# Kernel optimization log

Measured on AMD Instinct MI355X. Metric: run time of the kernel, lower is better.

Reference implementation:

```python
import jax, jax.numpy as jnp
import numpy as np
import math

IMAGE_SIZE = 256
VIEWING_ANGLE = 30.0  # degrees
NEAR = 0.1
FAR = 100.0
CHUNK = 50


def _look_at(vertices):
    # nr.look_at with at=origin, up=+y, eye from viewing_angle (as in __init__)
    eye = jnp.array([0.0, 0.0, -(1.0 / math.tan(math.radians(VIEWING_ANGLE)) + 1.0)],
                    dtype=vertices.dtype)
    at = jnp.zeros(3, dtype=vertices.dtype)
    up = jnp.array([0.0, 1.0, 0.0], dtype=vertices.dtype)
    z = at - eye
    z = z / jnp.linalg.norm(z)
    x = jnp.cross(up, z)
    x = x / jnp.linalg.norm(x)
    y = jnp.cross(z, x)
    y = y / jnp.linalg.norm(y)
    R = jnp.stack([x, y, z])  # [3,3] rows = camera axes
    return (vertices - eye) @ R.T


def _perspective(v):
    # nr.perspective: x,y divided by z*tan(angle); z (camera depth) kept
    width = math.tan(math.radians(VIEWING_ANGLE))
    z = v[..., 2]
    zs = jnp.where(jnp.abs(z) < 1e-5, 1e-5, z)  # avoid div-by-zero for behind-camera verts
    return jnp.stack([v[..., 0] / (zs * width), v[..., 1] / (zs * width), z], axis=-1)


def reference(vertices, faces):
    """Renderer.forward(vertices, faces, mode='depth'):
    fill_back -> look_at -> perspective -> vertices_to_faces -> rasterize_depth.
    Returns depth image [B, H, W] (FAR where no face covers the pixel)."""
    B = vertices.shape[0]
    # fill_back: append faces with reversed vertex order
    faces2 = jnp.concatenate([faces, faces[:, :, ::-1]], axis=1)  # [B, 2F, 3]
    v_scr = _perspective(_look_at(vertices))                      # [B, V, 3]
    # vertices_to_faces gather
    fv = jax.vmap(lambda v, f: v[f])(v_scr, faces2)               # [B, 2F, 3, 3]
    F2 = fv.shape[1]
    nsteps = F2 // CHUNK
    fv = fv.reshape(B, nsteps, CHUNK, 3, 3).transpose(1, 0, 2, 3, 4)  # [S,B,C,3,3]

    is_ = IMAGE_SIZE
    p = (2.0 * jnp.arange(is_, dtype=vertices.dtype) + 1.0 - is_) / is_  # pixel centers in (-1,1)
    py, px = jnp.meshgrid(p, p, indexing='ij')  # [H,W]

    def step(buf, f):  # f: [B,C,3,3]; z-buffer min over this face chunk
        x = f[..., 0][..., None, None]  # [B,C,3,1,1]
        y = f[..., 1][..., None, None]
        z = f[..., 2]                   # [B,C,3] camera-space depth per vertex
        x0, x1, x2 = x[:, :, 0], x[:, :, 1], x[:, :, 2]
        y0, y1, y2 = y[:, :, 0], y[:, :, 1], y[:, :, 2]
        area = (x1 - x0) * (y2 - y0) - (x2 - x0) * (y1 - y0)  # [B,C,1,1] signed 2*area
        area_s = jnp.where(jnp.abs(area) < 1e-8, 1e-8, area)
        # screen-space barycentric weights (edge functions / area)
        w0 = ((x1 - px) * (y2 - py) - (x2 - px) * (y1 - py)) / area_s
        w1 = ((x2 - px) * (y0 - py) - (x0 - px) * (y2 - py)) / area_s
        w2 = 1.0 - w0 - w1
        zc = jnp.maximum(z, 1e-4)  # safe for masked-out faces only
        # perspective-correct depth: z = 1 / (w0/z0 + w1/z1 + w2/z2)
        inv_z = (w0 / zc[:, :, 0, None, None] + w1 / zc[:, :, 1, None, None]
                 + w2 / zc[:, :, 2, None, None])
        zp = 1.0 / jnp.maximum(inv_z, 1e-6)
        front = jnp.all(z > NEAR, axis=-1)[..., None, None]
        inside = (w0 >= 0) & (w1 >= 0) & (w2 >= 0) & (jnp.abs(area) > 1e-8)
        valid = inside & front & (zp > NEAR) & (zp < FAR)
        zp = jnp.where(valid, zp, FAR)
        return jnp.minimum(buf, jnp.min(zp, axis=1)), None

    buf0 = jnp.full((B, is_, is_), FAR, dtype=vertices.dtype)
    depth, _ = jax.lax.scan(step, buf0, fv)
    return depth


def setup_inputs() -> dict:
    key = jax.random.key(0)
    kv, kf = jax.random.split(key)
    B, NV, NF = 1, 2502, 5000
    # mesh roughly within the camera frustum (eye at z~-2.73 looking at origin)
    vertices = 0.35 * jax.random.normal(kv, (B, NV, 3), dtype=jnp.float32)
    faces = jax.random.randint(kf, (B, NF, 3), 0, NV, dtype=jnp.int32)
    return {"vertices": vertices, "faces": faces}
```

## Files before the change

kernel.cpp:

```cpp
#include <hip/hip_runtime.h>
#include <hip/hip_bf16.h>

#define IS 256
#define NEARV 0.1f
#define FARV 100.0f
#define NTX 16
#define NTILES 256
#define CAP 5120
#define CHK 32
#define CPT ((CAP + CHK - 1) / CHK)
#define RBLOCKS 2048
#define RWAVES (RBLOCKS * 4)
#define MAXITEMS (NTILES * CPT)

__global__ void kinit(unsigned int* __restrict__ zb, int* __restrict__ count,
                      int* __restrict__ misc) {
    int i = blockIdx.x * 256 + threadIdx.x;
    zb[i] = 0x42C80000u;
    if (i < NTILES) count[i] = 0;
    if (i == NTILES) misc[0] = 0;
}

__launch_bounds__(256)
__global__ void kbinprep(const float* __restrict__ verts, const int* __restrict__ faces,
                         float4* __restrict__ fd, int* __restrict__ count,
                         unsigned short* __restrict__ list, int* __restrict__ misc,
                         int* __restrict__ items, int nf) {
    __shared__ int scnt[NTILES];
    __shared__ int sbase[NTILES];
    __shared__ int slast;
    const int tid = threadIdx.x;
    for (int t = tid; t < NTILES; t += 256) scnt[t] = 0;
    __syncthreads();

    const int f = blockIdx.x * 256 + tid;
    int kx0 = 0, kx1 = -1, ky0 = 0, ky1 = -1;
    float bxmin = 0.f, bymin = 0.f, bxmax = -1.f, bymax = -1.f;
    if (f < nf) {
        int i0 = faces[f * 3 + 0];
        int i1 = faces[f * 3 + 1];
        int i2 = faces[f * 3 + 2];
        float z0 = verts[i0 * 3 + 2] + 2.7320508075688772f;
        float z1 = verts[i1 * 3 + 2] + 2.7320508075688772f;
        float z2 = verts[i2 * 3 + 2] + 2.7320508075688772f;
        bool front = (z0 > NEARV) && (z1 > NEARV) && (z2 > NEARV);
        float zs0 = (fabsf(z0) < 1e-5f) ? 1e-5f : z0;
        float zs1 = (fabsf(z1) < 1e-5f) ? 1e-5f : z1;
        float zs2 = (fabsf(z2) < 1e-5f) ? 1e-5f : z2;
        float d0 = zs0 * 0.57735026918962576f;
        float d1 = zs1 * 0.57735026918962576f;
        float d2 = zs2 * 0.57735026918962576f;
        float x0 = verts[i0 * 3 + 0] / d0;
        float y0 = verts[i0 * 3 + 1] / d0;
        float x1 = verts[i1 * 3 + 0] / d1;
        float y1 = verts[i1 * 3 + 1] / d1;
        float x2 = verts[i2 * 3 + 0] / d2;
        float y2 = verts[i2 * 3 + 1] / d2;
        float area = (x1 - x0) * (y2 - y0) - (x2 - x0) * (y1 - y0);
        if (front && (fabsf(area) > 1e-8f)) {
            float xmin = fminf(x0, fminf(x1, x2));
            float xmax = fmaxf(x0, fmaxf(x1, x2));
            float ymin = fminf(y0, fminf(y1, y2));
            float ymax = fmaxf(y0, fmaxf(y1, y2));
            float ia = 1.0f / area;
            float iz0 = 1.0f / fmaxf(z0, 1e-4f);
            float iz1 = 1.0f / fmaxf(z1, 1e-4f);
            float iz2 = 1.0f / fmaxf(z2, 1e-4f);
            float4* o = fd + (size_t)f * 4;
            o[0] = make_float4(x0, y0, x1, y1);
            o[1] = make_float4(x2, y2, ia, iz0);
            o[2] = make_float4(iz1, iz2, 0.0f, 0.0f);
            bxmin = xmin; bymin = ymin; bxmax = xmax; bymax = ymax;
            float tminx = fminf(fmaxf((bxmin * 256.0f + 225.0f) * (1.0f / 32.0f), -2.0f), 17.0f);
            float tmaxx = fminf(fmaxf((bxmax * 256.0f + 255.0f) * (1.0f / 32.0f), -2.0f), 17.0f);
            float tminy = fminf(fmaxf((bymin * 256.0f + 225.0f) * (1.0f / 32.0f), -2.0f), 17.0f);
            float tmaxy = fminf(fmaxf((bymax * 256.0f + 255.0f) * (1.0f / 32.0f), -2.0f), 17.0f);
            kx0 = max(0, (int)ceilf(tminx) - 1);
            kx1 = min(NTX - 1, (int)floorf(tmaxx) + 1);
            ky0 = max(0, (int)ceilf(tminy) - 1);
            ky1 = min(NTX - 1, (int)floorf(tmaxy) + 1);
        }
    }
    for (int ky = ky0; ky <= ky1; ++ky) {
        float py_lo = (float)(32 * ky - 255) * (1.0f / 256.0f);
        float py_hi = (float)(32 * ky - 225) * (1.0f / 256.0f);
        if (!(bymin <= py_hi && bymax >= py_lo)) continue;
        for (int kx = kx0; kx <= kx1; ++kx) {
            float px_lo = (float)(32 * kx - 255) * (1.0f / 256.0f);
            float px_hi = (float)(32 * kx - 225) * (1.0f / 256.0f);
            if (bxmin <= px_hi && bxmax >= px_lo) atomicAdd(&scnt[ky * NTX + kx], 1);
        }
    }
    __syncthreads();
    for (int t = tid; t < NTILES; t += 256) {
        int c = scnt[t];
        sbase[t] = (c > 0) ? atomicAdd(&count[t], c) : 0;
        scnt[t] = 0;
    }
    __syncthreads();
    for (int ky = ky0; ky <= ky1; ++ky) {
        float py_lo = (float)(32 * ky - 255) * (1.0f / 256.0f);
        float py_hi = (float)(32 * ky - 225) * (1.0f / 256.0f);
        if (!(bymin <= py_hi && bymax >= py_lo)) continue;
        for (int kx = kx0; kx <= kx1; ++kx) {
            float px_lo = (float)(32 * kx - 255) * (1.0f / 256.0f);
            float px_hi = (float)(32 * kx - 225) * (1.0f / 256.0f);
            if (bxmin <= px_hi && bxmax >= px_lo) {
                int t = ky * NTX + kx;
                int slot = sbase[t] + atomicAdd(&scnt[t], 1);
                list[(size_t)t * CAP + slot] = (unsigned short)f;
            }
        }
    }
    __syncthreads();
    __threadfence();
    if (tid == 0) slast = (atomicAdd(&misc[0], 1) == (int)gridDim.x - 1) ? 1 : 0;
    __syncthreads();
    if (!slast) return;
    __threadfence();
    int c = __hip_atomic_load(&count[tid], __ATOMIC_RELAXED, __HIP_MEMORY_SCOPE_AGENT);
    int nch = (c + CHK - 1) / CHK;
    scnt[tid] = nch;
    __syncthreads();
    for (int d = 1; d < NTILES; d <<= 1) {
        int v = (tid >= d) ? scnt[tid - d] : 0;
        __syncthreads();
        scnt[tid] += v;
        __syncthreads();
    }
    int off = scnt[tid] - nch;
    if (tid == NTILES - 1) misc[64] = scnt[tid];
    for (int k = 0; k < nch; ++k) {
        int n = min(CHK, c - k * CHK);
        items[off + k] = (tid << 16) | (n << 8) | k;
    }
}

__launch_bounds__(256)
__global__ void kraster(const float4* __restrict__ fd, const unsigned int* __restrict__ list32,
                        const int* __restrict__ items, const int* __restrict__ misc,
                        unsigned int* __restrict__ zb) {
    const int wslot = __builtin_amdgcn_readfirstlane(threadIdx.x >> 6);
    const int wid = blockIdx.x * 4 + wslot;
    const int lane = threadIdx.x & 63;
    const int cx = lane & 15;
    const int ry = lane >> 4;
    const int ni = __builtin_amdgcn_readfirstlane(misc[64]);

    for (int it = wid; it < ni; it += RWAVES) {
        const int pk = __builtin_amdgcn_readfirstlane(items[it]);
        const int tile = pk >> 16;
        const int n = (pk >> 8) & 0xff;
        const int chunk = pk & 0xff;
        const int bx = tile & 15;
        const int by = tile >> 4;
        const int j = bx * 16 + cx;
        const float px = ((float)(2 * j + 1) - 256.0f) * (1.0f / 256.0f);
        float py[4];
        int row[4];
        unsigned int zcur[4];
#pragma unroll
        for (int r = 0; r < 4; ++r) {
            row[r] = by * 16 + ry + 4 * r;
            py[r] = ((float)(2 * row[r] + 1) - 256.0f) * (1.0f / 256.0f);
            zcur[r] = zb[row[r] * IS + j];
        }
        const unsigned int* lp32 = list32 + ((size_t)tile * CAP + chunk * CHK) / 2;

        float mx[4] = {0.0f, 0.0f, 0.0f, 0.0f};
        unsigned int pr = 0;

#pragma unroll 2
        for (int e = 0; e < n; ++e) {
            if ((e & 1) == 0)
                pr = (unsigned int)__builtin_amdgcn_readfirstlane((int)lp32[e >> 1]);
            const int fidx = (e & 1) ? (int)(pr >> 16) : (int)(pr & 0xffffu);
            const float4* p = fd + (size_t)fidx * 4;
            float4 a0 = p[0];
            float4 a1 = p[1];
            float4 a2 = p[2];
            float dx0 = a0.x - px, dx1 = a0.z - px, dx2 = a1.x - px;
#pragma unroll
            for (int r = 0; r < 4; ++r) {
                float dy0 = a0.y - py[r], dy1 = a0.w - py[r], dy2 = a1.y - py[r];
                float e0 = dx1 * dy2 - dx2 * dy1;
                float e1 = dx2 * dy0 - dx0 * dy2;
                float w0 = e0 * a1.z;
                float w1 = e1 * a1.z;
                float w2 = 1.0f - w0 - w1;
                float invz = w0 * a1.w + w1 * a2.x + w2 * a2.y;
                float invzc = fmaxf(invz, 1e-6f);
                float wmin = fminf(fminf(w0, w1), w2);
                bool ok = (wmin >= 0.0f) && (invzc < 10.0f) && (invzc > 0.01f);
                if (ok) mx[r] = fmaxf(mx[r], invzc);
            }
        }
#pragma unroll
        for (int r = 0; r < 4; ++r) {
            if (mx[r] > 0.0f) {
                float zp = 1.0f / mx[r];
                unsigned int zbits = __float_as_uint(zp);
                if (zbits < zcur[r]) atomicMin(&zb[row[r] * IS + j], zbits);
            }
        }
    }
}

extern "C" void kernel_launch(void* const* d_in, const int* in_sizes, int n_in,
                              void* d_out, int out_size, void* d_ws, size_t ws_size,
                              hipStream_t stream) {
    const float* verts = (const float*)d_in[0];
    const int* faces = (const int*)d_in[1];
    unsigned int* zb = (unsigned int*)d_out;

    const int nf = in_sizes[1] / 3;

    char* ws = (char*)d_ws;
    size_t off = 0;
    float4* fd = (float4*)(ws + off);            off += (size_t)nf * 64;
    off = (off + 255) & ~(size_t)255;
    int* count = (int*)(ws + off);               off += NTILES * 4;
    off = (off + 255) & ~(size_t)255;
    int* misc = (int*)(ws + off);                off += 512;
    int* items = (int*)(ws + off);               off += (size_t)MAXITEMS * 4;
    off = (off + 255) & ~(size_t)255;
    unsigned short* list = (unsigned short*)(ws + off);

    const int nb = (nf + 255) / 256;

    kinit<<<(IS * IS) / 256, 256, 0, stream>>>(zb, count, misc);
    kbinprep<<<nb, 256, 0, stream>>>(verts, faces, fd, count, list, misc, items, nf);
    kraster<<<RBLOCKS, 256, 0, stream>>>(fd, (const unsigned int*)list, items, misc, zb);
}
```

Baseline: 110.9 us.

## Replace global atomics and last-block scan with per-segment bin lists

Merges the z-buffer init kernel into the prep kernel and drops the global per-tile atomic counters, the last-block detection and the prefix scan that built the work-item list. Each block now writes its per-tile counts to a tile×segment table and fills a fixed 256-entry slot region per segment. The raster kernel then walks a fixed grid of tile×slot work units, with an XOR swizzle, and skips empty ones. This removes one launch and the serialized tail in binning, at the cost of scanning many empty work slots and using sparser list storage.

```diff
diff --git a/kernel.cpp b/kernel.cpp
--- a/kernel.cpp
+++ b/kernel.cpp
@@ -1,39 +1,33 @@
 #include <hip/hip_runtime.h>
-#include <hip/hip_bf16.h>
 
 #define IS 256
 #define NEARV 0.1f
 #define FARV 100.0f
 #define NTX 16
 #define NTILES 256
-#define CAP 5120
+#define SEGSZ 256
+#define NSEGMAX 20
+#define CAP (SEGSZ * NSEGMAX)
 #define CHK 32
-#define CPT ((CAP + CHK - 1) / CHK)
 #define RBLOCKS 2048
 #define RWAVES (RBLOCKS * 4)
-#define MAXITEMS (NTILES * CPT)
-
-__global__ void kinit(unsigned int* __restrict__ zb, int* __restrict__ count,
-                      int* __restrict__ misc) {
-    int i = blockIdx.x * 256 + threadIdx.x;
-    zb[i] = 0x42C80000u;
-    if (i < NTILES) count[i] = 0;
-    if (i == NTILES) misc[0] = 0;
-}
+#define NSLOTS (NTILES * 256)
 
 __launch_bounds__(256)
-__global__ void kbinprep(const float* __restrict__ verts, const int* __restrict__ faces,
-                         float4* __restrict__ fd, int* __restrict__ count,
-                         unsigned short* __restrict__ list, int* __restrict__ misc,
-                         int* __restrict__ items, int nf) {
+__global__ void kprep(const float* __restrict__ verts, const int* __restrict__ faces,
+                      float4* __restrict__ fd, int* __restrict__ cnt2,
+                      unsigned short* __restrict__ list, unsigned int* __restrict__ zb,
+                      int nf, int nseg) {
     __shared__ int scnt[NTILES];
-    __shared__ int sbase[NTILES];
-    __shared__ int slast;
     const int tid = threadIdx.x;
-    for (int t = tid; t < NTILES; t += 256) scnt[t] = 0;
+    const int bid = blockIdx.x;
+    zb[bid * 256 + tid] = 0x42C80000u;
+    if (bid >= nseg) return;
+
+    scnt[tid] = 0;
     __syncthreads();
 
-    const int f = blockIdx.x * 256 + tid;
+    const int f = bid * 256 + tid;
     int kx0 = 0, kx1 = -1, ky0 = 0, ky1 = -1;
     float bxmin = 0.f, bymin = 0.f, bxmax = -1.f, bymax = -1.f;
     if (f < nf) {
@@ -58,10 +52,10 @@
         float y2 = verts[i2 * 3 + 1] / d2;
         float area = (x1 - x0) * (y2 - y0) - (x2 - x0) * (y1 - y0);
         if (front && (fabsf(area) > 1e-8f)) {
-            float xmin = fminf(x0, fminf(x1, x2));
-            float xmax = fmaxf(x0, fmaxf(x1, x2));
-            float ymin = fminf(y0, fminf(y1, y2));
-            float ymax = fmaxf(y0, fmaxf(y1, y2));
+            bxmin = fminf(x0, fminf(x1, x2));
+            bxmax = fmaxf(x0, fmaxf(x1, x2));
+            bymin = fminf(y0, fminf(y1, y2));
+            bymax = fmaxf(y0, fmaxf(y1, y2));
             float ia = 1.0f / area;
             float iz0 = 1.0f / fmaxf(z0, 1e-4f);
             float iz1 = 1.0f / fmaxf(z1, 1e-4f);
@@ -70,7 +64,6 @@
             o[0] = make_float4(x0, y0, x1, y1);
             o[1] = make_float4(x2, y2, ia, iz0);
             o[2] = make_float4(iz1, iz2, 0.0f, 0.0f);
-            bxmin = xmin; bymin = ymin; bxmax = xmax; bymax = ymax;
             float tminx = fminf(fmaxf((bxmin * 256.0f + 225.0f) * (1.0f / 32.0f), -2.0f), 17.0f);
             float tmaxx = fminf(fmaxf((bxmax * 256.0f + 255.0f) * (1.0f / 32.0f), -2.0f), 17.0f);
             float tminy = fminf(fmaxf((bymin * 256.0f + 225.0f) * (1.0f / 32.0f), -2.0f), 17.0f);
@@ -92,11 +85,8 @@
         }
     }
     __syncthreads();
-    for (int t = tid; t < NTILES; t += 256) {
-        int c = scnt[t];
-        sbase[t] = (c > 0) ? atomicAdd(&count[t], c) : 0;
-        scnt[t] = 0;
-    }
+    cnt2[tid * nseg + bid] = scnt[tid];
+    scnt[tid] = 0;
     __syncthreads();
     for (int ky = ky0; ky <= ky1; ++ky) {
         float py_lo = (float)(32 * ky - 255) * (1.0f / 256.0f);
@@ -107,51 +97,34 @@
             float px_hi = (float)(32 * kx - 225) * (1.0f / 256.0f);
             if (bxmin <= px_hi && bxmax >= px_lo) {
                 int t = ky * NTX + kx;
-                int slot = sbase[t] + atomicAdd(&scnt[t], 1);
-                list[(size_t)t * CAP + slot] = (unsigned short)f;
+                int slot = atomicAdd(&scnt[t], 1);
+                list[(size_t)t * CAP + bid * SEGSZ + slot] = (unsigned short)f;
             }
         }
-    }
-    __syncthreads();
-    __threadfence();
-    if (tid == 0) slast = (atomicAdd(&misc[0], 1) == (int)gridDim.x - 1) ? 1 : 0;
-    __syncthreads();
-    if (!slast) return;
-    __threadfence();
-    int c = __hip_atomic_load(&count[tid], __ATOMIC_RELAXED, __HIP_MEMORY_SCOPE_AGENT);
-    int nch = (c + CHK - 1) / CHK;
-    scnt[tid] = nch;
-    __syncthreads();
-    for (int d = 1; d < NTILES; d <<= 1) {
-        int v = (tid >= d) ? scnt[tid - d] : 0;
-        __syncthreads();
-        scnt[tid] += v;
-        __syncthreads();
-    }
-    int off = scnt[tid] - nch;
-    if (tid == NTILES - 1) misc[64] = scnt[tid];
-    for (int k = 0; k < nch; ++k) {
-        int n = min(CHK, c - k * CHK);
-        items[off + k] = (tid << 16) | (n << 8) | k;
     }
 }
 
 __launch_bounds__(256)
 __global__ void kraster(const float4* __restrict__ fd, const unsigned int* __restrict__ list32,
-                        const int* __restrict__ items, const int* __restrict__ misc,
-                        unsigned int* __restrict__ zb) {
+                        const int* __restrict__ cnt2, unsigned int* __restrict__ zb,
+                        int nseg) {
     const int wslot = __builtin_amdgcn_readfirstlane(threadIdx.x >> 6);
     const int wid = blockIdx.x * 4 + wslot;
     const int lane = threadIdx.x & 63;
     const int cx = lane & 15;
     const int ry = lane >> 4;
-    const int ni = __builtin_amdgcn_readfirstlane(misc[64]);
-
-    for (int it = wid; it < ni; it += RWAVES) {
-        const int pk = __builtin_amdgcn_readfirstlane(items[it]);
-        const int tile = pk >> 16;
-        const int n = (pk >> 8) & 0xff;
-        const int chunk = pk & 0xff;
+
+    for (int w = wid; w < NSLOTS; w += RWAVES) {
+        const int tile = w >> 8;
+        const int slot = (w & 255) ^ tile;
+        const int seg = slot >> 3;
+        if (seg >= nseg) continue;
+        const int c = cnt2[tile * nseg + seg];
+        const int k = slot & 7;
+        const int n0 = c - k * CHK;
+        if (n0 <= 0) continue;
+        const int n = min(CHK, n0);
+
         const int bx = tile & 15;
         const int by = tile >> 4;
         const int j = bx * 16 + cx;
@@ -165,7 +138,7 @@
             py[r] = ((float)(2 * row[r] + 1) - 256.0f) * (1.0f / 256.0f);
             zcur[r] = zb[row[r] * IS + j];
         }
-        const unsigned int* lp32 = list32 + ((size_t)tile * CAP + chunk * CHK) / 2;
+        const unsigned int* lp32 = list32 + ((size_t)tile * CAP + seg * SEGSZ + k * CHK) / 2;
 
         float mx[4] = {0.0f, 0.0f, 0.0f, 0.0f};
         unsigned int pr = 0;
@@ -214,21 +187,16 @@
     unsigned int* zb = (unsigned int*)d_out;
 
     const int nf = in_sizes[1] / 3;
+    const int nseg = (nf + SEGSZ - 1) / SEGSZ;
 
     char* ws = (char*)d_ws;
     size_t off = 0;
-    float4* fd = (float4*)(ws + off);            off += (size_t)nf * 64;
+    float4* fd = (float4*)(ws + off);     off += (size_t)nf * 64;
     off = (off + 255) & ~(size_t)255;
-    int* count = (int*)(ws + off);               off += NTILES * 4;
-    off = (off + 255) & ~(size_t)255;
-    int* misc = (int*)(ws + off);                off += 512;
-    int* items = (int*)(ws + off);               off += (size_t)MAXITEMS * 4;
+    int* cnt2 = (int*)(ws + off);         off += (size_t)NTILES * NSEGMAX * 4;
     off = (off + 255) & ~(size_t)255;
     unsigned short* list = (unsigned short*)(ws + off);
 
-    const int nb = (nf + 255) / 256;
-
-    kinit<<<(IS * IS) / 256, 256, 0, stream>>>(zb, count, misc);
-    kbinprep<<<nb, 256, 0, stream>>>(verts, faces, fd, count, list, misc, items, nf);
-    kraster<<<RBLOCKS, 256, 0, stream>>>(fd, (const unsigned int*)list, items, misc, zb);
+    kprep<<<256, 256, 0, stream>>>(verts, faces, fd, cnt2, list, zb, nf, nseg);
+    kraster<<<RBLOCKS, 256, 0, stream>>>(fd, (const unsigned int*)list, cnt2, zb, nseg);
 }
```

Result: slower. 131.9 us (+18.9%).
